# Optimization experiments

Measured on AMD Instinct MI355X. Metric: run time of the kernel, lower is better.

The kernel has to match this reference:

```python
import jax, jax.numpy as jnp
import numpy as np

N_HEAD = 8
D_MODEL = 512
D_K = 512
D_V = 512
D_KH = D_K // N_HEAD
D_VH = D_V // N_HEAD
EPS = 1e-6


def setup_inputs() -> dict:
    key = jax.random.key(0)
    ks = jax.random.split(key, 10)
    B, L = 16, 1024
    q = jax.random.normal(ks[0], (B, L, D_MODEL), dtype=jnp.float32)
    k = jax.random.normal(ks[1], (B, L, D_MODEL), dtype=jnp.float32)
    v = jax.random.normal(ks[2], (B, L, D_MODEL), dtype=jnp.float32)
    mask = jax.random.randint(ks[3], (B, L, L), 0, 2).astype(bool)
    s = 1.0 / np.sqrt(D_MODEL)
    Wq = jax.random.normal(ks[4], (D_MODEL, D_K), dtype=jnp.float32) * s
    Wk = jax.random.normal(ks[5], (D_MODEL, D_K), dtype=jnp.float32) * s
    Wv = jax.random.normal(ks[6], (D_MODEL, D_V), dtype=jnp.float32) * s
    Wfc = jax.random.normal(ks[7], (D_V, D_MODEL), dtype=jnp.float32) * (1.0 / np.sqrt(D_V))
    gamma = jnp.ones((D_MODEL,), dtype=jnp.float32)
    beta = jnp.zeros((D_MODEL,), dtype=jnp.float32)
    return {"q": q, "k": k, "v": v, "mask": mask, "Wq": Wq, "Wk": Wk,
            "Wv": Wv, "Wfc": Wfc, "gamma": gamma, "beta": beta}


def reference(q, k, v, mask, Wq, Wk, Wv, Wfc, gamma, beta):
    B, Lq, _ = q.shape
    Lk = k.shape[1]
    residual = q
    # projections -> [B, H, L, d_head]
    qh = (q @ Wq).reshape(B, Lq, N_HEAD, D_KH).transpose(0, 2, 1, 3)
    kh = (k @ Wk).reshape(B, Lk, N_HEAD, D_KH).transpose(0, 2, 1, 3)
    vh = (v @ Wv).reshape(B, Lk, N_HEAD, D_VH).transpose(0, 2, 1, 3)
    # scaled dot-product attention; scale uses per-head dim (source rebinds d_k)
    scores = jnp.einsum('bhqd,bhkd->bhqk', qh / np.sqrt(D_KH), kh)
    scores = jnp.where(mask[:, None, :, :], -1e9, scores)
    attn = jax.nn.softmax(scores, axis=-1)
    out = jnp.einsum('bhqk,bhkd->bhqd', attn, vh)
    out = out.transpose(0, 2, 1, 3).reshape(B, Lq, D_V)
    out = out @ Wfc + residual
    # layer norm
    mu = jnp.mean(out, axis=-1, keepdims=True)
    var = jnp.var(out, axis=-1, keepdims=True)
    out = (out - mu) * jax.lax.rsqrt(var + EPS) * gamma + beta
    return out, attn
```

## Files before the change

### kernel.cpp

```cpp
#include <hip/hip_runtime.h>
#include <hip/hip_bf16.h>

typedef __attribute__((ext_vector_type(8))) short s8v;
typedef __attribute__((ext_vector_type(4))) short s4v;
typedef __attribute__((ext_vector_type(4))) float f4v;

__device__ __forceinline__ short f2bf(float f){
  unsigned u = __builtin_bit_cast(unsigned, f);
  u += 0x7fffu + ((u >> 16) & 1u);
  return (short)(u >> 16);
}

__device__ __forceinline__ f4v mfma16(s8v a, s8v b, f4v c){
  return __builtin_amdgcn_mfma_f32_16x16x32_bf16(a, b, c, 0, 0, 0);
}

__global__ __launch_bounds__(256) void prep_kernel(
    const int* __restrict__ mask, unsigned* __restrict__ bits,
    const float* __restrict__ Wq, const float* __restrict__ Wk,
    const float* __restrict__ Wv, const float* __restrict__ Wfc,
    short* __restrict__ Wt)
{
  if (blockIdx.x < 2048){
    const int lane = threadIdx.x & 63;
    const int wid = blockIdx.x*4 + (threadIdx.x >> 6);
    for (int i = 0; i < 32; ++i){
      const int c = wid*32 + i;
      int mv = __builtin_nontemporal_load(&mask[(size_t)c*64 + lane]);
      unsigned long long bal = __ballot(mv != 0);
      if (lane == 0)  bits[c*2]   = (unsigned)bal;
      if (lane == 32) bits[c*2+1] = (unsigned)(bal >> 32);
    }
  } else {
    const int bid = blockIdx.x - 2048;
    const int w = bid >> 10;
    const float* __restrict__ W = (w==0)?Wq:(w==1)?Wk:(w==2)?Wv:Wfc;
    const int idx = (bid & 1023)*256 + threadIdx.x;
    const int kk = idx >> 9, n = idx & 511;
    Wt[w*262144 + n*512 + kk] = f2bf(W[idx]);
  }
}

__global__ __launch_bounds__(256) void proj_kernel(
    const float* __restrict__ qin, const float* __restrict__ kin,
    const float* __restrict__ vin, const short* __restrict__ Wt,
    short* __restrict__ Qh, short* __restrict__ Kh, short* __restrict__ Vt)
{
  const int work = (blockIdx.x & 7)*384 + (blockIdx.x >> 3);
  const int z = work >> 10;
  const int r = work & 1023;
  const int mt = r >> 2, nt = r & 3;
  const float* __restrict__ A = (z==0) ? qin : (z==1) ? kin : vin;
  const short* __restrict__ W = Wt + z*262144;
  const int m0 = mt*64, n0 = nt*128;
  __shared__ __align__(16) short Alds[64*40];
  const int tid = threadIdx.x, lane = tid & 63, wave = tid >> 6;
  const int wm = wave >> 1, wn = wave & 1;
  const int col = lane & 15, kg = lane >> 4;
  f4v acc[2][4];
  #pragma unroll
  for (int i=0;i<2;i++)
    #pragma unroll
    for (int j=0;j<4;j++) acc[i][j] = (f4v){0.f,0.f,0.f,0.f};

  const int arow = tid >> 2, aoff = (tid & 3)*8;
  const float* Ap = A + (size_t)(m0 + arow)*512 + aoff;
  short* Aw = &Alds[arow*40 + aoff];

  for (int k0 = 0; k0 < 512; k0 += 32){
    float4 x0 = *(const float4*)(Ap + k0);
    float4 x1 = *(const float4*)(Ap + k0 + 4);
    s8v ab;
    ab[0]=f2bf(x0.x); ab[1]=f2bf(x0.y); ab[2]=f2bf(x0.z); ab[3]=f2bf(x0.w);
    ab[4]=f2bf(x1.x); ab[5]=f2bf(x1.y); ab[6]=f2bf(x1.z); ab[7]=f2bf(x1.w);
    __syncthreads();
    *(s8v*)Aw = ab;
    __syncthreads();
    s8v af0 = *(const s8v*)&Alds[(wm*32 + col)*40 + kg*8];
    s8v af1 = *(const s8v*)&Alds[(wm*32 + 16 + col)*40 + kg*8];
    #pragma unroll
    for (int f=0; f<4; f++){
      const int n = n0 + wn*64 + f*16 + col;
      s8v bf = *(const s8v*)(W + n*512 + k0 + kg*8);
      acc[0][f] = mfma16(af0, bf, acc[0][f]);
      acc[1][f] = mfma16(af1, bf, acc[1][f]);
    }
  }
  const float scale = (z==0) ? 0.125f : 1.0f;
  #pragma unroll
  for (int fr=0; fr<2; fr++)
    #pragma unroll
    for (int f=0; f<4; f++)
      #pragma unroll
      for (int j=0; j<4; j++){
        int rr = m0 + wm*32 + fr*16 + kg*4 + j;
        int c = n0 + wn*64 + f*16 + col;
        int b = rr >> 10, l = rr & 1023, hh = c >> 6, d = c & 63;
        short val = f2bf(acc[fr][f][j] * scale);
        if (z==0)      Qh[((size_t)(b*8+hh)*1024 + l)*64 + d] = val;
        else if (z==1) Kh[((size_t)(b*8+hh)*1024 + l)*64 + d] = val;
        else           Vt[((size_t)(b*8+hh)*64 + d)*1024 + l] = val;
      }
}

__global__ __launch_bounds__(256) void attn_kernel(
  const short* __restrict__ Qh, const short* __restrict__ Kh,
  const short* __restrict__ Vt, const unsigned* __restrict__ bits,
  float* __restrict__ attn, short* __restrict__ ctx)
{
  const int work = ((blockIdx.x & 7) << 8) | (blockIdx.x >> 3);
  const int bh = work >> 4;
  const int q0 = (work & 15) * 64;
  const int b = bh >> 3, h = bh & 7;
  __shared__ unsigned mb[64*33];
  __shared__ __align__(16) short Pb[64*128];
  __shared__ float red[256];
  __shared__ float rowinv[64];
  const int tid = threadIdx.x, lane = tid & 63, wave = tid >> 6;
  const int col = lane & 15, kg = lane >> 4;
  const short* Qb = Qh + (size_t)bh*65536;
  const short* Kb = Kh + (size_t)bh*65536;
  const short* Vb = Vt + (size_t)bh*65536;
  const f4v zf = (f4v){0.f,0.f,0.f,0.f};

  {
    const int r = tid >> 2, w = (tid & 3)*8;
    const unsigned* src = bits + (size_t)(b*1024 + q0 + r)*32 + w;
    uint4 w0 = *(const uint4*)src;
    uint4 w1 = *(const uint4*)(src + 4);
    unsigned* dst = &mb[r*33 + w];
    dst[0]=w0.x; dst[1]=w0.y; dst[2]=w0.z; dst[3]=w0.w;
    dst[4]=w1.x; dst[5]=w1.y; dst[6]=w1.z; dst[7]=w1.w;
  }

  s8v qf[4][2];
  #pragma unroll
  for (int qi = 0; qi < 4; ++qi)
    #pragma unroll
    for (int ks = 0; ks < 2; ++ks)
      qf[qi][ks] = *(const s8v*)(Qb + (q0 + qi*16 + col)*64 + ks*32 + kg*8);

  __syncthreads();

  float sum[4] = {0.f, 0.f, 0.f, 0.f};
  for (int it = 0; it < 8; ++it){
    const int c0 = it*128 + wave*32;
    unsigned mw[4];
    #pragma unroll
    for (int qi = 0; qi < 4; ++qi) mw[qi] = mb[(qi*16 + col)*33 + (c0>>5)];
    #pragma unroll
    for (int ch = 0; ch < 2; ++ch){
      const short* kp = Kb + (c0 + ch*16 + col)*64 + kg*8;
      s8v kf0 = *(const s8v*)kp;
      s8v kf1 = *(const s8v*)(kp + 32);
      #pragma unroll
      for (int qi = 0; qi < 4; ++qi){
        f4v a = mfma16(kf0, qf[qi][0], zf);
        a = mfma16(kf1, qf[qi][1], a);
        #pragma unroll
        for (int j = 0; j < 4; ++j){
          const int bit = ch*16 + kg*4 + j;
          float e = __expf(a[j]);
          sum[qi] += ((mw[qi]>>bit)&1) ? 0.f : e;
        }
      }
    }
  }
  #pragma unroll
  for (int qi = 0; qi < 4; ++qi){
    sum[qi] += __shfl_xor(sum[qi], 16);
    sum[qi] += __shfl_xor(sum[qi], 32);
  }
  if (kg == 0){
    #pragma unroll
    for (int qi = 0; qi < 4; ++qi) red[wave*64 + qi*16 + col] = sum[qi];
  }
  __syncthreads();
  if (tid < 64)
    rowinv[tid] = 1.0f / (red[tid] + red[64+tid] + red[128+tid] + red[192+tid]);
  __syncthreads();
  float inv[4];
  #pragma unroll
  for (int qi = 0; qi < 4; ++qi) inv[qi] = rowinv[qi*16 + col];

  f4v cacc[4] = {zf, zf, zf, zf};
  const int d0 = wave*16;
  float* ab = attn + (size_t)(bh*1024 + q0)*1024;
  const int sw = (col & 7) << 3;
  for (int it = 0; it < 8; ++it){
    const int c0 = it*128 + wave*32;
    unsigned mw[4];
    #pragma unroll
    for (int qi = 0; qi < 4; ++qi) mw[qi] = mb[(qi*16 + col)*33 + (c0>>5)];
    #pragma unroll
    for (int ch = 0; ch < 2; ++ch){
      const int cc = c0 + ch*16;
      const short* kp = Kb + (cc + col)*64 + kg*8;
      s8v kf0 = *(const s8v*)kp;
      s8v kf1 = *(const s8v*)(kp + 32);
      #pragma unroll
      for (int qi = 0; qi < 4; ++qi){
        f4v a = mfma16(kf0, qf[qi][0], zf);
        a = mfma16(kf1, qf[qi][1], a);
        f4v p; s4v pk;
        #pragma unroll
        for (int j = 0; j < 4; ++j){
          const int bit = ch*16 + kg*4 + j;
          float e = __expf(a[j]) * inv[qi];
          p[j] = ((mw[qi]>>bit)&1) ? 0.f : e;
          pk[j] = f2bf(p[j]);
        }
        __builtin_nontemporal_store(p,
            (f4v*)(ab + (size_t)(qi*16 + col)*1024 + cc + kg*4));
        *(s4v*)&Pb[(qi*16 + col)*128 + ((wave*32 + ch*16 + kg*4) ^ sw)] = pk;
      }
    }
    __syncthreads();
    #pragma unroll
    for (int sub = 0; sub < 4; ++sub){
      s8v vf = *(const s8v*)(Vb + (size_t)(d0 + col)*1024 + it*128 + sub*32 + kg*8);
      const int kr = (sub*32 + kg*8) ^ sw;
      #pragma unroll
      for (int qi = 0; qi < 4; ++qi){
        s8v pa = *(const s8v*)&Pb[(qi*16 + col)*128 + kr];
        cacc[qi] = mfma16(pa, vf, cacc[qi]);
      }
    }
    __syncthreads();
  }

  short* cb = ctx + (size_t)(b*1024 + q0)*512 + h*64 + d0 + col;
  #pragma unroll
  for (int qi = 0; qi < 4; ++qi)
    #pragma unroll
    for (int j = 0; j < 4; ++j)
      cb[(size_t)(qi*16 + kg*4 + j)*512] = f2bf(cacc[qi][j]);
}

__global__ __launch_bounds__(256) void outproj_ln_kernel(
  const short* __restrict__ ctx, const short* __restrict__ Wf,
  const float* __restrict__ resid, const float* __restrict__ gamma,
  const float* __restrict__ beta, float* __restrict__ out)
{
  const int m0 = blockIdx.x * 32;
  __shared__ __align__(16) short Alds[32*40];
  __shared__ float sred[32*4], qred[32*4];
  __shared__ float mLds[32], rLds[32];
  const int tid = threadIdx.x, lane = tid & 63, wave = tid >> 6;
  const int col = lane & 15, kg = lane >> 4;
  const int n0 = wave * 128;

  f4v acc[2][8];
  #pragma unroll
  for (int mf=0; mf<2; mf++)
    #pragma unroll
    for (int nf=0; nf<8; nf++) acc[mf][nf] = (f4v){0.f,0.f,0.f,0.f};

  const int arow = tid >> 3, ac = (tid & 7)*4;
  const short* Ap = ctx + (size_t)(m0 + arow)*512 + ac;
  short* Aw = &Alds[arow*40 + ac];

  for (int k0 = 0; k0 < 512; k0 += 32){
    s4v av = *(const s4v*)(Ap + k0);
    __syncthreads();
    *(s4v*)Aw = av;
    __syncthreads();
    s8v af[2];
    #pragma unroll
    for (int mf=0; mf<2; mf++)
      af[mf] = *(const s8v*)&Alds[(mf*16 + col)*40 + kg*8];
    #pragma unroll
    for (int nf=0; nf<8; nf++){
      s8v bf = *(const s8v*)(Wf + (size_t)(n0 + nf*16 + col)*512 + k0 + kg*8);
      #pragma unroll
      for (int mf=0; mf<2; mf++)
        acc[mf][nf] = mfma16(af[mf], bf, acc[mf][nf]);
    }
  }

  float g[8], bt[8];
  #pragma unroll
  for (int nf=0; nf<8; nf++){
    g[nf]  = gamma[n0 + nf*16 + col];
    bt[nf] = beta[n0 + nf*16 + col];
  }

  #pragma unroll
  for (int mf=0; mf<2; mf++)
    #pragma unroll
    for (int j=0; j<4; j++){
      const int rl = mf*16 + kg*4 + j;
      const size_t r = (size_t)(m0 + rl);
      float s = 0.f, qq = 0.f;
      #pragma unroll
      for (int nf=0; nf<8; nf++){
        float y = acc[mf][nf][j] + resid[r*512 + n0 + nf*16 + col];
        acc[mf][nf][j] = y;
        s += y; qq += y*y;
      }
      #pragma unroll
      for (int d=1; d<16; d<<=1){ s += __shfl_xor(s, d); qq += __shfl_xor(qq, d); }
      if (col == 0){ sred[rl*4 + wave] = s; qred[rl*4 + wave] = qq; }
    }
  __syncthreads();
  if (tid < 32){
    float S = sred[tid*4] + sred[tid*4+1] + sred[tid*4+2] + sred[tid*4+3];
    float Q = qred[tid*4] + qred[tid*4+1] + qred[tid*4+2] + qred[tid*4+3];
    float mean = S * (1.0f/512.0f);
    float var  = Q * (1.0f/512.0f) - mean*mean;
    mLds[tid] = mean;
    rLds[tid] = rsqrtf(var + 1e-6f);
  }
  __syncthreads();

  #pragma unroll
  for (int mf=0; mf<2; mf++)
    #pragma unroll
    for (int j=0; j<4; j++){
      const int rl = mf*16 + kg*4 + j;
      const size_t r = (size_t)(m0 + rl);
      const float mean = mLds[rl], rs = rLds[rl];
      #pragma unroll
      for (int nf=0; nf<8; nf++)
        out[r*512 + n0 + nf*16 + col] = (acc[mf][nf][j] - mean)*rs*g[nf] + bt[nf];
    }
}

extern "C" void kernel_launch(void* const* d_in, const int* in_sizes, int n_in,
                              void* d_out, int out_size, void* d_ws, size_t ws_size,
                              hipStream_t stream) {
  const float* q    = (const float*)d_in[0];
  const float* k    = (const float*)d_in[1];
  const float* v    = (const float*)d_in[2];
  const int*   mask = (const int*)d_in[3];
  const float* Wq   = (const float*)d_in[4];
  const float* Wk   = (const float*)d_in[5];
  const float* Wv   = (const float*)d_in[6];
  const float* Wfc  = (const float*)d_in[7];
  const float* gamma= (const float*)d_in[8];
  const float* beta = (const float*)d_in[9];

  char* ws = (char*)d_ws;
  short* Wt  = (short*)(ws);
  short* Qh  = (short*)(ws + ((size_t)2<<20));
  short* Kh  = (short*)(ws + ((size_t)18<<20));
  short* Vt  = (short*)(ws + ((size_t)34<<20));
  short* ctx = (short*)(ws + ((size_t)50<<20));

  float* out  = (float*)d_out;
  float* attn = out + (size_t)16384*512;
  unsigned* bits = (unsigned*)d_out;

  prep_kernel<<<dim3(6144,1,1), 256, 0, stream>>>(mask, bits, Wq, Wk, Wv, Wfc, Wt);
  proj_kernel <<<dim3(3072,1,1), 256, 0, stream>>>(q, k, v, Wt, Qh, Kh, Vt);
  attn_kernel <<<dim3(2048,1,1), 256, 0, stream>>>(Qh, Kh, Vt, bits, attn, ctx);
  outproj_ln_kernel<<<dim3(512,1,1), 256, 0, stream>>>(ctx, Wt + 3*262144, q,
                                                       gamma, beta, out);
}
```

Baseline: 394.5 us.

## Fuse mask bit-packing into projection, drop LDS staging, transpose V via LDS

```diff
diff --git a/kernel.cpp b/kernel.cpp
--- a/kernel.cpp
+++ b/kernel.cpp
@@ -15,15 +15,27 @@
   return __builtin_amdgcn_mfma_f32_16x16x32_bf16(a, b, c, 0, 0, 0);
 }
 
-__global__ __launch_bounds__(256) void prep_kernel(
-    const int* __restrict__ mask, unsigned* __restrict__ bits,
+__global__ __launch_bounds__(256) void transpose_w(
     const float* __restrict__ Wq, const float* __restrict__ Wk,
     const float* __restrict__ Wv, const float* __restrict__ Wfc,
     short* __restrict__ Wt)
 {
-  if (blockIdx.x < 2048){
+  const int w = blockIdx.x >> 10;
+  const float* __restrict__ W = (w==0)?Wq:(w==1)?Wk:(w==2)?Wv:Wfc;
+  const int idx = (blockIdx.x & 1023)*256 + threadIdx.x;
+  const int kk = idx >> 9, n = idx & 511;
+  Wt[w*262144 + n*512 + kk] = f2bf(W[idx]);
+}
+
+__global__ __launch_bounds__(256) void proj_kernel(
+    const float* __restrict__ qin, const float* __restrict__ kin,
+    const float* __restrict__ vin, const short* __restrict__ Wt,
+    const int* __restrict__ mask, unsigned* __restrict__ bits,
+    short* __restrict__ Qh, short* __restrict__ Kh, short* __restrict__ Vt)
+{
+  if (blockIdx.x >= 3072){
     const int lane = threadIdx.x & 63;
-    const int wid = blockIdx.x*4 + (threadIdx.x >> 6);
+    const int wid = (blockIdx.x - 3072)*4 + (threadIdx.x >> 6);
     for (int i = 0; i < 32; ++i){
       const int c = wid*32 + i;
       int mv = __builtin_nontemporal_load(&mask[(size_t)c*64 + lane]);
@@ -31,21 +43,8 @@
       if (lane == 0)  bits[c*2]   = (unsigned)bal;
       if (lane == 32) bits[c*2+1] = (unsigned)(bal >> 32);
     }
-  } else {
-    const int bid = blockIdx.x - 2048;
-    const int w = bid >> 10;
-    const float* __restrict__ W = (w==0)?Wq:(w==1)?Wk:(w==2)?Wv:Wfc;
-    const int idx = (bid & 1023)*256 + threadIdx.x;
-    const int kk = idx >> 9, n = idx & 511;
-    Wt[w*262144 + n*512 + kk] = f2bf(W[idx]);
-  }
-}
-
-__global__ __launch_bounds__(256) void proj_kernel(
-    const float* __restrict__ qin, const float* __restrict__ kin,
-    const float* __restrict__ vin, const short* __restrict__ Wt,
-    short* __restrict__ Qh, short* __restrict__ Kh, short* __restrict__ Vt)
-{
+    return;
+  }
   const int work = (blockIdx.x & 7)*384 + (blockIdx.x >> 3);
   const int z = work >> 10;
   const int r = work & 1023;
@@ -53,54 +52,75 @@
   const float* __restrict__ A = (z==0) ? qin : (z==1) ? kin : vin;
   const short* __restrict__ W = Wt + z*262144;
   const int m0 = mt*64, n0 = nt*128;
-  __shared__ __align__(16) short Alds[64*40];
+  __shared__ __align__(16) short Tlds[128*68];
   const int tid = threadIdx.x, lane = tid & 63, wave = tid >> 6;
   const int wm = wave >> 1, wn = wave & 1;
   const int col = lane & 15, kg = lane >> 4;
+
   f4v acc[2][4];
   #pragma unroll
   for (int i=0;i<2;i++)
     #pragma unroll
     for (int j=0;j<4;j++) acc[i][j] = (f4v){0.f,0.f,0.f,0.f};
 
-  const int arow = tid >> 2, aoff = (tid & 3)*8;
-  const float* Ap = A + (size_t)(m0 + arow)*512 + aoff;
-  short* Aw = &Alds[arow*40 + aoff];
+  const float* Ap0 = A + (size_t)(m0 + wm*32 + col)*512 + kg*8;
+  const float* Ap1 = Ap0 + (size_t)16*512;
+  const short* Wp  = W + (size_t)(n0 + wn*64 + col)*512 + kg*8;
 
   for (int k0 = 0; k0 < 512; k0 += 32){
-    float4 x0 = *(const float4*)(Ap + k0);
-    float4 x1 = *(const float4*)(Ap + k0 + 4);
-    s8v ab;
-    ab[0]=f2bf(x0.x); ab[1]=f2bf(x0.y); ab[2]=f2bf(x0.z); ab[3]=f2bf(x0.w);
-    ab[4]=f2bf(x1.x); ab[5]=f2bf(x1.y); ab[6]=f2bf(x1.z); ab[7]=f2bf(x1.w);
-    __syncthreads();
-    *(s8v*)Aw = ab;
-    __syncthreads();
-    s8v af0 = *(const s8v*)&Alds[(wm*32 + col)*40 + kg*8];
-    s8v af1 = *(const s8v*)&Alds[(wm*32 + 16 + col)*40 + kg*8];
+    float4 x0 = *(const float4*)(Ap0 + k0);
+    float4 x1 = *(const float4*)(Ap0 + k0 + 4);
+    float4 y0 = *(const float4*)(Ap1 + k0);
+    float4 y1 = *(const float4*)(Ap1 + k0 + 4);
+    s8v af0, af1;
+    af0[0]=f2bf(x0.x); af0[1]=f2bf(x0.y); af0[2]=f2bf(x0.z); af0[3]=f2bf(x0.w);
+    af0[4]=f2bf(x1.x); af0[5]=f2bf(x1.y); af0[6]=f2bf(x1.z); af0[7]=f2bf(x1.w);
+    af1[0]=f2bf(y0.x); af1[1]=f2bf(y0.y); af1[2]=f2bf(y0.z); af1[3]=f2bf(y0.w);
+    af1[4]=f2bf(y1.x); af1[5]=f2bf(y1.y); af1[6]=f2bf(y1.z); af1[7]=f2bf(y1.w);
     #pragma unroll
     for (int f=0; f<4; f++){
-      const int n = n0 + wn*64 + f*16 + col;
-      s8v bf = *(const s8v*)(W + n*512 + k0 + kg*8);
+      s8v bf = *(const s8v*)(Wp + (size_t)f*16*512 + k0);
       acc[0][f] = mfma16(af0, bf, acc[0][f]);
       acc[1][f] = mfma16(af1, bf, acc[1][f]);
     }
   }
-  const float scale = (z==0) ? 0.125f : 1.0f;
-  #pragma unroll
-  for (int fr=0; fr<2; fr++)
-    #pragma unroll
-    for (int f=0; f<4; f++)
-      #pragma unroll
-      for (int j=0; j<4; j++){
-        int rr = m0 + wm*32 + fr*16 + kg*4 + j;
-        int c = n0 + wn*64 + f*16 + col;
-        int b = rr >> 10, l = rr & 1023, hh = c >> 6, d = c & 63;
-        short val = f2bf(acc[fr][f][j] * scale);
-        if (z==0)      Qh[((size_t)(b*8+hh)*1024 + l)*64 + d] = val;
-        else if (z==1) Kh[((size_t)(b*8+hh)*1024 + l)*64 + d] = val;
-        else           Vt[((size_t)(b*8+hh)*64 + d)*1024 + l] = val;
-      }
+
+  if (z < 2){
+    const float scale = (z==0) ? 0.125f : 1.0f;
+    short* D = (z==0) ? Qh : Kh;
+    #pragma unroll
+    for (int fr=0; fr<2; fr++)
+      #pragma unroll
+      for (int f=0; f<4; f++)
+        #pragma unroll
+        for (int j=0; j<4; j++){
+          int rr = m0 + wm*32 + fr*16 + kg*4 + j;
+          int c = n0 + wn*64 + f*16 + col;
+          int b = rr >> 10, l = rr & 1023, hh = c >> 6, d = c & 63;
+          D[((size_t)(b*8+hh)*1024 + l)*64 + d] = f2bf(acc[fr][f][j] * scale);
+        }
+  } else {
+    #pragma unroll
+    for (int fr=0; fr<2; fr++)
+      #pragma unroll
+      for (int f=0; f<4; f++)
+        #pragma unroll
+        for (int j=0; j<4; j++){
+          const int rl = wm*32 + fr*16 + kg*4 + j;
+          const int cl = wn*64 + f*16 + col;
+          Tlds[cl*68 + rl] = f2bf(acc[fr][f][j]);
+        }
+    __syncthreads();
+    const int b = m0 >> 10, lbase = m0 & 1023;
+    #pragma unroll
+    for (int it=0; it<4; ++it){
+      const int idx = it*256 + tid;
+      const int cl = idx >> 3, rc = idx & 7;
+      const int c = n0 + cl, hh = c >> 6, d = c & 63;
+      s8v vv = *(const s8v*)&Tlds[cl*68 + rc*8];
+      *(s8v*)(Vt + ((size_t)(b*8+hh)*64 + d)*1024 + lbase + rc*8) = vv;
+    }
+  }
 }
 
 __global__ __launch_bounds__(256) void attn_kernel(
@@ -242,39 +262,26 @@
   const float* __restrict__ resid, const float* __restrict__ gamma,
   const float* __restrict__ beta, float* __restrict__ out)
 {
-  const int m0 = blockIdx.x * 32;
-  __shared__ __align__(16) short Alds[32*40];
-  __shared__ float sred[32*4], qred[32*4];
-  __shared__ float mLds[32], rLds[32];
+  const int m0 = blockIdx.x * 16;
+  __shared__ float sred[16*4], qred[16*4];
+  __shared__ float mLds[16], rLds[16];
   const int tid = threadIdx.x, lane = tid & 63, wave = tid >> 6;
   const int col = lane & 15, kg = lane >> 4;
   const int n0 = wave * 128;
 
-  f4v acc[2][8];
-  #pragma unroll
-  for (int mf=0; mf<2; mf++)
-    #pragma unroll
-    for (int nf=0; nf<8; nf++) acc[mf][nf] = (f4v){0.f,0.f,0.f,0.f};
-
-  const int arow = tid >> 3, ac = (tid & 7)*4;
-  const short* Ap = ctx + (size_t)(m0 + arow)*512 + ac;
-  short* Aw = &Alds[arow*40 + ac];
+  f4v acc[8];
+  #pragma unroll
+  for (int nf=0; nf<8; nf++) acc[nf] = (f4v){0.f,0.f,0.f,0.f};
+
+  const short* Ap = ctx + (size_t)(m0 + col)*512 + kg*8;
+  const short* Wp = Wf + (size_t)(n0 + col)*512 + kg*8;
 
   for (int k0 = 0; k0 < 512; k0 += 32){
-    s4v av = *(const s4v*)(Ap + k0);
-    __syncthreads();
-    *(s4v*)Aw = av;
-    __syncthreads();
-    s8v af[2];
-    #pragma unroll
-    for (int mf=0; mf<2; mf++)
-      af[mf] = *(const s8v*)&Alds[(mf*16 + col)*40 + kg*8];
+    s8v af = *(const s8v*)(Ap + k0);
     #pragma unroll
     for (int nf=0; nf<8; nf++){
-      s8v bf = *(const s8v*)(Wf + (size_t)(n0 + nf*16 + col)*512 + k0 + kg*8);
-      #pragma unroll
-      for (int mf=0; mf<2; mf++)
-        acc[mf][nf] = mfma16(af[mf], bf, acc[mf][nf]);
+      s8v bf = *(const s8v*)(Wp + (size_t)nf*16*512 + k0);
+      acc[nf] = mfma16(af, bf, acc[nf]);
     }
   }
 
@@ -286,24 +293,22 @@
   }
 
   #pragma unroll
-  for (int mf=0; mf<2; mf++)
-    #pragma unroll
-    for (int j=0; j<4; j++){
-      const int rl = mf*16 + kg*4 + j;
-      const size_t r = (size_t)(m0 + rl);
-      float s = 0.f, qq = 0.f;
-      #pragma unroll
-      for (int nf=0; nf<8; nf++){
-        float y = acc[mf][nf][j] + resid[r*512 + n0 + nf*16 + col];
-        acc[mf][nf][j] = y;
-        s += y; qq += y*y;
-      }
-      #pragma unroll
-      for (int d=1; d<16; d<<=1){ s += __shfl_xor(s, d); qq += __shfl_xor(qq, d); }
-      if (col == 0){ sred[rl*4 + wave] = s; qred[rl*4 + wave] = qq; }
-    }
-  __syncthreads();
-  if (tid < 32){
+  for (int j=0; j<4; j++){
+    const int rl = kg*4 + j;
+    const size_t r = (size_t)(m0 + rl);
+    float s = 0.f, qq = 0.f;
+    #pragma unroll
+    for (int nf=0; nf<8; nf++){
+      float y = acc[nf][j] + resid[r*512 + n0 + nf*16 + col];
+      acc[nf][j] = y;
+      s += y; qq += y*y;
+    }
+    #pragma unroll
+    for (int d=1; d<16; d<<=1){ s += __shfl_xor(s, d); qq += __shfl_xor(qq, d); }
+    if (col == 0){ sred[rl*4 + wave] = s; qred[rl*4 + wave] = qq; }
+  }
+  __syncthreads();
+  if (tid < 16){
     float S = sred[tid*4] + sred[tid*4+1] + sred[tid*4+2] + sred[tid*4+3];
     float Q = qred[tid*4] + qred[tid*4+1] + qred[tid*4+2] + qred[tid*4+3];
     float mean = S * (1.0f/512.0f);
@@ -314,16 +319,14 @@
   __syncthreads();
 
   #pragma unroll
-  for (int mf=0; mf<2; mf++)
-    #pragma unroll
-    for (int j=0; j<4; j++){
-      const int rl = mf*16 + kg*4 + j;
-      const size_t r = (size_t)(m0 + rl);
-      const float mean = mLds[rl], rs = rLds[rl];
-      #pragma unroll
-      for (int nf=0; nf<8; nf++)
-        out[r*512 + n0 + nf*16 + col] = (acc[mf][nf][j] - mean)*rs*g[nf] + bt[nf];
-    }
+  for (int j=0; j<4; j++){
+    const int rl = kg*4 + j;
+    const size_t r = (size_t)(m0 + rl);
+    const float mean = mLds[rl], rs = rLds[rl];
+    #pragma unroll
+    for (int nf=0; nf<8; nf++)
+      out[r*512 + n0 + nf*16 + col] = (acc[nf][j] - mean)*rs*g[nf] + bt[nf];
+  }
 }
 
 extern "C" void kernel_launch(void* const* d_in, const int* in_sizes, int n_in,
@@ -351,9 +354,10 @@
   float* attn = out + (size_t)16384*512;
   unsigned* bits = (unsigned*)d_out;
 
-  prep_kernel<<<dim3(6144,1,1), 256, 0, stream>>>(mask, bits, Wq, Wk, Wv, Wfc, Wt);
-  proj_kernel <<<dim3(3072,1,1), 256, 0, stream>>>(q, k, v, Wt, Qh, Kh, Vt);
+  transpose_w <<<dim3(4096,1,1), 256, 0, stream>>>(Wq, Wk, Wv, Wfc, Wt);
+  proj_kernel <<<dim3(5120,1,1), 256, 0, stream>>>(q, k, v, Wt, mask, bits,
+                                                   Qh, Kh, Vt);
   attn_kernel <<<dim3(2048,1,1), 256, 0, stream>>>(Qh, Kh, Vt, bits, attn, ctx);
-  outproj_ln_kernel<<<dim3(512,1,1), 256, 0, stream>>>(ctx, Wt + 3*262144, q,
-                                                       gamma, beta, out);
-}
+  outproj_ln_kernel<<<dim3(1024,1,1), 256, 0, stream>>>(ctx, Wt + 3*262144, q,
+                                                        gamma, beta, out);
+}
```

Result: slower. 472.2 us (+19.7%).
